# Kernel tuning notes

Hardware: AMD Instinct MI355X
Metric: run time of the kernel (lower is better)

Reference implementation:

```python
import jax, jax.numpy as jnp
import numpy as np

B, K, N, F = 32, 4, 512, 128


def setup_inputs() -> dict:
    key = jax.random.key(0)
    k1, k2, k3, k4 = jax.random.split(key, 4)
    H = jax.random.normal(k1, (B, N, F), dtype=jnp.float32)
    E = jax.random.uniform(k2, (B, K, N, N), dtype=jnp.float32)
    # xavier_normal_ equivalents
    rw_std = float(np.sqrt(2.0 / (F + F * K)))  # torch xavier treats last dims
    RW = jax.random.normal(k3, (F, F, K), dtype=jnp.float32) * rw_std
    sw_std = float(np.sqrt(2.0 / (F + F)))
    SW = jax.random.normal(k4, (F, F), dtype=jnp.float32) * sw_std
    return {"H": H, "E": E, "RW": RW, "SW": SW}


def reference(H, E, RW, SW):
    # D = 1 / sum over (k, i) of (E + I)  -> [b, n]
    n = E.shape[2]
    D = 1.0 / (E + jnp.eye(n, dtype=E.dtype)).sum(axis=(1, 2))  # [b, n]
    # relational aggregation: sum_{k,j,m} E[b,k,i,j] H[b,j,m] RW[m,f,k] -> [b,i,f]
    rel = jnp.einsum('bkij,bjm,mfk->bif', E, H, RW)
    self_term = jnp.einsum('bjf,fl->bjl', H, SW)
    return jax.nn.sigmoid(D[:, :, None] * rel + self_term)
```

## Files before the change

### kernel.cpp

```cpp
#include <hip/hip_runtime.h>
#include <hip/hip_bf16.h>

#define B_ 32
#define K_ 4
#define N_ 512
#define F_ 128

typedef __attribute__((ext_vector_type(8))) short short8;
typedef __attribute__((ext_vector_type(4))) short short4v;
typedef __attribute__((ext_vector_type(4))) float float4v;

__device__ __forceinline__ unsigned short f2bf(float x) {
    unsigned int u = __builtin_bit_cast(unsigned int, x);
    u += 0x7FFFu + ((u >> 16) & 1u);
    return (unsigned short)(u >> 16);
}

__device__ __forceinline__ short8 pack8(float4v a, float4v b) {
    short8 r;
    r[0] = (short)f2bf(a[0]); r[1] = (short)f2bf(a[1]);
    r[2] = (short)f2bf(a[2]); r[3] = (short)f2bf(a[3]);
    r[4] = (short)f2bf(b[0]); r[5] = (short)f2bf(b[1]);
    r[6] = (short)f2bf(b[2]); r[7] = (short)f2bf(b[3]);
    return r;
}

__global__ void k0_weights(const float* __restrict__ RW, const float* __restrict__ SW,
                           unsigned short* __restrict__ Wt, unsigned short* __restrict__ SWt) {
    int r = blockIdx.x;
    int m = threadIdx.x;
    if (r < 512) {
        int k = r >> 7, f = r & 127;
        Wt[r * F_ + m] = f2bf(RW[(m * F_ + f) * K_ + k]);
    } else {
        int l = r - 512;
        SWt[l * F_ + m] = f2bf(SW[m * F_ + l]);
    }
}

__global__ void k1v2_convert(const float* __restrict__ E, float* __restrict__ colsum,
                             unsigned short* __restrict__ Ebf) {
    int bid = blockIdx.x;
    int b   = bid >> 5;
    int isl = (bid >> 1) & 15;
    int jt  = bid & 1;
    int t   = threadIdx.x;
    int j   = jt * 256 + (t & 63) * 4;
    int r0  = isl * 32 + (t >> 6) * 8;

    float cs0 = 0.f, cs1 = 0.f, cs2 = 0.f, cs3 = 0.f;
#pragma unroll
    for (int k = 0; k < K_; ++k) {
        const float* Ep = E + ((size_t)((b * K_ + k) * N_ + r0)) * N_ + j;
        unsigned short* Op = Ebf + ((size_t)((b * K_ + k) * N_ + r0)) * N_ + j;
#pragma unroll
        for (int r = 0; r < 8; ++r) {
            float4v v = *(const float4v*)(Ep + (size_t)r * N_);
            cs0 += v[0]; cs1 += v[1]; cs2 += v[2]; cs3 += v[3];
            short4v s;
            s[0] = (short)f2bf(v[0]); s[1] = (short)f2bf(v[1]);
            s[2] = (short)f2bf(v[2]); s[3] = (short)f2bf(v[3]);
            *(short4v*)(Op + (size_t)r * N_) = s;
        }
    }
    atomicAdd(&colsum[b * N_ + j + 0], cs0);
    atomicAdd(&colsum[b * N_ + j + 1], cs1);
    atomicAdd(&colsum[b * N_ + j + 2], cs2);
    atomicAdd(&colsum[b * N_ + j + 3], cs3);
}

__global__ void k2_expand(const float* __restrict__ H, const unsigned short* __restrict__ Wt,
                          unsigned short* __restrict__ Tt) {
    int bid = blockIdx.x;
    int b  = bid >> 5;
    int ct = (bid >> 2) & 7;
    int jt = bid & 3;
    int lane = threadIdx.x & 63;
    int wv   = threadIdx.x >> 6;
    int c0 = ct * 64 + wv * 16;
    int jbase = jt * 128;
    int lrow = lane & 15, lgrp = lane >> 4;

    float4v acc[8];
#pragma unroll
    for (int i = 0; i < 8; ++i) acc[i] = {0.f, 0.f, 0.f, 0.f};

#pragma unroll
    for (int ms = 0; ms < 4; ++ms) {
        int m0 = ms * 32;
        short8 a = *(const short8*)(Wt + (c0 + lrow) * F_ + m0 + lgrp * 8);
#pragma unroll
        for (int cf = 0; cf < 8; ++cf) {
            int j = jbase + cf * 16 + lrow;
            const float* hp = H + ((size_t)b * N_ + j) * F_ + m0 + lgrp * 8;
            float4v h0 = *(const float4v*)hp;
            float4v h1 = *(const float4v*)(hp + 4);
            short8 bb = pack8(h0, h1);
            acc[cf] = __builtin_amdgcn_mfma_f32_16x16x32_bf16(a, bb, acc[cf], 0, 0, 0);
        }
    }
#pragma unroll
    for (int cf = 0; cf < 8; ++cf) {
#pragma unroll
        for (int r = 0; r < 4; ++r) {
            int c = c0 + lgrp * 4 + r;
            int j = jbase + cf * 16 + lrow;
            Tt[((size_t)b * 512 + c) * N_ + j] = f2bf(acc[cf][r]);
        }
    }
}

__global__ void __launch_bounds__(512)
k3v2_rel(const unsigned short* __restrict__ Ebf, const unsigned short* __restrict__ Tt,
         float* __restrict__ relP) {
    int bid = blockIdx.x;
    int b  = bid >> 4;
    int it = (bid >> 1) & 7;
    int jc = bid & 1;
    int lane = threadIdx.x & 63;
    int wv   = threadIdx.x >> 6;
    int i0 = it * 64 + (wv >> 1) * 16;
    int f0 = (wv & 1) * 64;
    int lrow = lane & 15, lgrp = lane >> 4;
    int jbase = jc * 256;

    float4v acc[4];
#pragma unroll
    for (int i = 0; i < 4; ++i) acc[i] = {0.f, 0.f, 0.f, 0.f};

    const unsigned short* Eb = Ebf + ((size_t)(b * K_) * N_ + (i0 + lrow)) * N_ + jbase + lgrp * 8;
    const unsigned short* Tb = Tt + ((size_t)b * 512 + f0 + lrow) * N_ + jbase + lgrp * 8;

#define EA(t) (const short8*)(Eb + ((t) >> 3) * 262144 + ((t) & 7) * 32)
#define TA(t, cf) (const short8*)(Tb + ((t) >> 3) * 65536 + (cf) * 8192 + ((t) & 7) * 32)

    short8 a0, b00, b01, b02, b03;
    short8 a1, b10, b11, b12, b13;
    a0 = *EA(0); b00 = *TA(0, 0); b01 = *TA(0, 1); b02 = *TA(0, 2); b03 = *TA(0, 3);

    for (int t = 0; t < 32; t += 2) {
        int t1 = t + 1;
        int t2 = (t + 2 < 32) ? t + 2 : 31;
        a1 = *EA(t1); b10 = *TA(t1, 0); b11 = *TA(t1, 1); b12 = *TA(t1, 2); b13 = *TA(t1, 3);
        acc[0] = __builtin_amdgcn_mfma_f32_16x16x32_bf16(a0, b00, acc[0], 0, 0, 0);
        acc[1] = __builtin_amdgcn_mfma_f32_16x16x32_bf16(a0, b01, acc[1], 0, 0, 0);
        acc[2] = __builtin_amdgcn_mfma_f32_16x16x32_bf16(a0, b02, acc[2], 0, 0, 0);
        acc[3] = __builtin_amdgcn_mfma_f32_16x16x32_bf16(a0, b03, acc[3], 0, 0, 0);
        a0 = *EA(t2); b00 = *TA(t2, 0); b01 = *TA(t2, 1); b02 = *TA(t2, 2); b03 = *TA(t2, 3);
        acc[0] = __builtin_amdgcn_mfma_f32_16x16x32_bf16(a1, b10, acc[0], 0, 0, 0);
        acc[1] = __builtin_amdgcn_mfma_f32_16x16x32_bf16(a1, b11, acc[1], 0, 0, 0);
        acc[2] = __builtin_amdgcn_mfma_f32_16x16x32_bf16(a1, b12, acc[2], 0, 0, 0);
        acc[3] = __builtin_amdgcn_mfma_f32_16x16x32_bf16(a1, b13, acc[3], 0, 0, 0);
    }
#undef EA
#undef TA

    float* dst = relP + (size_t)jc * (B_ * N_ * F_);
#pragma unroll
    for (int cf = 0; cf < 4; ++cf) {
#pragma unroll
        for (int r = 0; r < 4; ++r) {
            int i = i0 + lgrp * 4 + r;
            int f = f0 + cf * 16 + lrow;
            dst[((size_t)b * N_ + i) * F_ + f] = acc[cf][r];
        }
    }
}

__global__ void __launch_bounds__(512)
k4_epi(const float* __restrict__ relP, const float* __restrict__ H,
       const unsigned short* __restrict__ SWt, const float* __restrict__ colsum,
       float* __restrict__ out) {
    int bid = blockIdx.x;
    int b  = bid >> 3;
    int it = bid & 7;
    int lane = threadIdx.x & 63;
    int wv   = threadIdx.x >> 6;
    int i0 = it * 64 + (wv >> 1) * 16;
    int f0 = (wv & 1) * 64;
    int lrow = lane & 15, lgrp = lane >> 4;

    float4v accS[4];
#pragma unroll
    for (int i = 0; i < 4; ++i) accS[i] = {0.f, 0.f, 0.f, 0.f};

    const float* Hp = H + ((size_t)b * N_ + i0 + lrow) * F_;
#pragma unroll
    for (int ms = 0; ms < 4; ++ms) {
        int m0 = ms * 32;
        const float* hp = Hp + m0 + lgrp * 8;
        float4v h0 = *(const float4v*)hp;
        float4v h1 = *(const float4v*)(hp + 4);
        short8 a = pack8(h0, h1);
#pragma unroll
        for (int cf = 0; cf < 4; ++cf) {
            const unsigned short* sp = SWt + (f0 + cf * 16 + lrow) * F_ + m0 + lgrp * 8;
            short8 bb = *(const short8*)sp;
            accS[cf] = __builtin_amdgcn_mfma_f32_16x16x32_bf16(a, bb, accS[cf], 0, 0, 0);
        }
    }

    float Dv[4];
#pragma unroll
    for (int r = 0; r < 4; ++r) {
        int i = i0 + lgrp * 4 + r;
        Dv[r] = 1.0f / (colsum[b * N_ + i] + (float)K_);
    }
#pragma unroll
    for (int cf = 0; cf < 4; ++cf) {
#pragma unroll
        for (int r = 0; r < 4; ++r) {
            int i = i0 + lgrp * 4 + r;
            int f = f0 + cf * 16 + lrow;
            size_t idx = ((size_t)b * N_ + i) * F_ + f;
            float v = relP[idx] + relP[idx + (size_t)B_ * N_ * F_];
            float x = Dv[r] * v + accS[cf][r];
            out[idx] = 1.0f / (1.0f + __expf(-x));
        }
    }
}

__global__ void k1_colsum(const float* __restrict__ E, float* __restrict__ colsum) {
    int bid = blockIdx.x;
    int b   = bid >> 5;
    int jt  = (bid >> 4) & 1;
    int isl = bid & 15;
    int j   = jt * 256 + threadIdx.x;
    int i0  = isl * 32;
    float s0 = 0.f, s1 = 0.f, s2 = 0.f, s3 = 0.f;
#pragma unroll
    for (int k = 0; k < K_; ++k) {
        const float* p = E + ((size_t)((b * K_ + k) * N_ + i0)) * N_ + j;
#pragma unroll 4
        for (int ii = 0; ii < 32; ii += 4) {
            s0 += p[(ii + 0) * N_];
            s1 += p[(ii + 1) * N_];
            s2 += p[(ii + 2) * N_];
            s3 += p[(ii + 3) * N_];
        }
    }
    atomicAdd(&colsum[b * N_ + j], (s0 + s1) + (s2 + s3));
}

__global__ void __launch_bounds__(512)
k3_fuse(const float* __restrict__ E, const float* __restrict__ H,
        const unsigned short* __restrict__ Tt, const unsigned short* __restrict__ SWt,
        const float* __restrict__ colsum, float* __restrict__ out) {
    int bid = blockIdx.x;
    int b  = bid >> 3;
    int it = bid & 7;
    int lane = threadIdx.x & 63;
    int wv   = threadIdx.x >> 6;
    int i0 = it * 64 + (wv >> 1) * 16;
    int f0 = (wv & 1) * 64;
    int lrow = lane & 15, lgrp = lane >> 4;

    float4v accR[4], accS[4];
#pragma unroll
    for (int i = 0; i < 4; ++i) { accR[i] = {0.f, 0.f, 0.f, 0.f}; accS[i] = {0.f, 0.f, 0.f, 0.f}; }

    for (int k = 0; k < K_; ++k) {
        const float* Eb = E + ((size_t)((b * K_ + k) * N_ + i0 + lrow)) * N_;
        const unsigned short* Tb = Tt + ((size_t)b * 512 + k * 128 + f0) * N_;
#pragma unroll 2
        for (int js = 0; js < 16; ++js) {
            int j0 = js * 32;
            const float* ep = Eb + j0 + lgrp * 8;
            float4v e0 = *(const float4v*)ep;
            float4v e1 = *(const float4v*)(ep + 4);
            short8 a = pack8(e0, e1);
#pragma unroll
            for (int cf = 0; cf < 4; ++cf) {
                const unsigned short* tp = Tb + (size_t)(cf * 16 + lrow) * N_ + j0 + lgrp * 8;
                short8 bb = *(const short8*)tp;
                accR[cf] = __builtin_amdgcn_mfma_f32_16x16x32_bf16(a, bb, accR[cf], 0, 0, 0);
            }
        }
    }
    {
        const float* Hp = H + ((size_t)b * N_ + i0 + lrow) * F_;
#pragma unroll
        for (int ms = 0; ms < 4; ++ms) {
            int m0 = ms * 32;
            const float* hp = Hp + m0 + lgrp * 8;
            float4v h0 = *(const float4v*)hp;
            float4v h1 = *(const float4v*)(hp + 4);
            short8 a = pack8(h0, h1);
#pragma unroll
            for (int cf = 0; cf < 4; ++cf) {
                const unsigned short* sp = SWt + (f0 + cf * 16 + lrow) * F_ + m0 + lgrp * 8;
                short8 bb = *(const short8*)sp;
                accS[cf] = __builtin_amdgcn_mfma_f32_16x16x32_bf16(a, bb, accS[cf], 0, 0, 0);
            }
        }
    }
    float Dv[4];
#pragma unroll
    for (int r = 0; r < 4; ++r) {
        int i = i0 + lgrp * 4 + r;
        Dv[r] = 1.0f / (colsum[b * N_ + i] + (float)K_);
    }
#pragma unroll
    for (int cf = 0; cf < 4; ++cf) {
#pragma unroll
        for (int r = 0; r < 4; ++r) {
            int i = i0 + lgrp * 4 + r;
            int f = f0 + cf * 16 + lrow;
            float x = Dv[r] * accR[cf][r] + accS[cf][r];
            out[((size_t)b * N_ + i) * F_ + f] = 1.0f / (1.0f + __expf(-x));
        }
    }
}

extern "C" void kernel_launch(void* const* d_in, const int* in_sizes, int n_in,
                              void* d_out, int out_size, void* d_ws, size_t ws_size,
                              hipStream_t stream) {
    const float* H  = (const float*)d_in[0];
    const float* E  = (const float*)d_in[1];
    const float* RW = (const float*)d_in[2];
    const float* SW = (const float*)d_in[3];
    float* out = (float*)d_out;

    char* ws = (char*)d_ws;
    unsigned short* Wt  = (unsigned short*)(ws);
    unsigned short* SWt = (unsigned short*)(ws + 131072);
    float* colsum       = (float*)(ws + 163840);
    unsigned short* Tt  = (unsigned short*)(ws + 262144);
    unsigned short* Ebf = (unsigned short*)(ws + 17039360);
    float* relP         = (float*)(ws + 84148224);
    const size_t WS_NEED = 100925440ull;

    hipMemsetAsync(colsum, 0, B_ * N_ * sizeof(float), stream);
    k0_weights<<<640, 128, 0, stream>>>(RW, SW, Wt, SWt);

    if (ws_size >= WS_NEED) {
        k1v2_convert<<<1024, 256, 0, stream>>>(E, colsum, Ebf);
        k2_expand<<<1024, 256, 0, stream>>>(H, Wt, Tt);
        k3v2_rel<<<512, 512, 0, stream>>>(Ebf, Tt, relP);
        k4_epi<<<256, 512, 0, stream>>>(relP, H, SWt, colsum, out);
    } else {
        k1_colsum<<<1024, 256, 0, stream>>>(E, colsum);
        k2_expand<<<1024, 256, 0, stream>>>(H, Wt, Tt);
        k3_fuse<<<256, 512, 0, stream>>>(E, H, Tt, SWt, colsum, out);
    }
}
```

Before: 339.8 us.

## Widen E conversion per thread, split rel GEMM over four j-chunks

Result: no change. 342.2 us (+0.7%).

```diff
diff --git a/kernel.cpp b/kernel.cpp
--- a/kernel.cpp
+++ b/kernel.cpp
@@ -38,39 +38,59 @@
     }
 }
 
-__global__ void k1v2_convert(const float* __restrict__ E, float* __restrict__ colsum,
-                             unsigned short* __restrict__ Ebf) {
-    int bid = blockIdx.x;
-    int b   = bid >> 5;
-    int isl = (bid >> 1) & 15;
-    int jt  = bid & 1;
+__global__ void __launch_bounds__(256)
+k1v3_convert(const float* __restrict__ E, float* __restrict__ colsum,
+             unsigned short* __restrict__ Ebf) {
+    int bid = blockIdx.x;
+    int b   = bid >> 6;
+    int k   = (bid >> 4) & 3;
+    int isl = bid & 15;
     int t   = threadIdx.x;
-    int j   = jt * 256 + (t & 63) * 4;
+    int j8  = (t & 63) * 8;
     int r0  = isl * 32 + (t >> 6) * 8;
 
-    float cs0 = 0.f, cs1 = 0.f, cs2 = 0.f, cs3 = 0.f;
-#pragma unroll
-    for (int k = 0; k < K_; ++k) {
-        const float* Ep = E + ((size_t)((b * K_ + k) * N_ + r0)) * N_ + j;
-        unsigned short* Op = Ebf + ((size_t)((b * K_ + k) * N_ + r0)) * N_ + j;
-#pragma unroll
-        for (int r = 0; r < 8; ++r) {
-            float4v v = *(const float4v*)(Ep + (size_t)r * N_);
-            cs0 += v[0]; cs1 += v[1]; cs2 += v[2]; cs3 += v[3];
-            short4v s;
-            s[0] = (short)f2bf(v[0]); s[1] = (short)f2bf(v[1]);
-            s[2] = (short)f2bf(v[2]); s[3] = (short)f2bf(v[3]);
-            *(short4v*)(Op + (size_t)r * N_) = s;
-        }
-    }
-    atomicAdd(&colsum[b * N_ + j + 0], cs0);
-    atomicAdd(&colsum[b * N_ + j + 1], cs1);
-    atomicAdd(&colsum[b * N_ + j + 2], cs2);
-    atomicAdd(&colsum[b * N_ + j + 3], cs3);
-}
-
-__global__ void k2_expand(const float* __restrict__ H, const unsigned short* __restrict__ Wt,
-                          unsigned short* __restrict__ Tt) {
+    const size_t base = ((size_t)((b * K_ + k) * N_ + r0)) * N_ + j8;
+    const float* Ep = E + base;
+    unsigned short* Op = Ebf + base;
+
+    float4v va[8], vb[8];
+#pragma unroll
+    for (int r = 0; r < 4; ++r) {
+        va[r] = *(const float4v*)(Ep + (size_t)r * N_);
+        vb[r] = *(const float4v*)(Ep + (size_t)r * N_ + 4);
+    }
+#pragma unroll
+    for (int r = 4; r < 8; ++r) {
+        va[r] = *(const float4v*)(Ep + (size_t)r * N_);
+        vb[r] = *(const float4v*)(Ep + (size_t)r * N_ + 4);
+    }
+
+    float cs[8];
+#pragma unroll
+    for (int e = 0; e < 8; ++e) cs[e] = 0.f;
+#pragma unroll
+    for (int r = 0; r < 8; ++r) {
+        cs[0] += va[r][0]; cs[1] += va[r][1]; cs[2] += va[r][2]; cs[3] += va[r][3];
+        cs[4] += vb[r][0]; cs[5] += vb[r][1]; cs[6] += vb[r][2]; cs[7] += vb[r][3];
+        *(short8*)(Op + (size_t)r * N_) = pack8(va[r], vb[r]);
+    }
+
+    __shared__ float red[256][9];
+#pragma unroll
+    for (int e = 0; e < 8; ++e) red[t][e] = cs[e];
+    __syncthreads();
+    if (t < 64) {
+#pragma unroll
+        for (int e = 0; e < 8; ++e) {
+            float s = red[t][e] + red[t + 64][e] + red[t + 128][e] + red[t + 192][e];
+            atomicAdd(&colsum[b * N_ + t * 8 + e], s);
+        }
+    }
+}
+
+__global__ void __launch_bounds__(256)
+k2v2_expand(const float* __restrict__ H, const unsigned short* __restrict__ Wt,
+            unsigned short* __restrict__ Tt) {
     int bid = blockIdx.x;
     int b  = bid >> 5;
     int ct = (bid >> 2) & 7;
@@ -89,13 +109,16 @@
     for (int ms = 0; ms < 4; ++ms) {
         int m0 = ms * 32;
         short8 a = *(const short8*)(Wt + (c0 + lrow) * F_ + m0 + lgrp * 8);
+        float4v hv0[8], hv1[8];
 #pragma unroll
         for (int cf = 0; cf < 8; ++cf) {
-            int j = jbase + cf * 16 + lrow;
-            const float* hp = H + ((size_t)b * N_ + j) * F_ + m0 + lgrp * 8;
-            float4v h0 = *(const float4v*)hp;
-            float4v h1 = *(const float4v*)(hp + 4);
-            short8 bb = pack8(h0, h1);
+            const float* hp = H + ((size_t)b * N_ + jbase + cf * 16 + lrow) * F_ + m0 + lgrp * 8;
+            hv0[cf] = *(const float4v*)hp;
+            hv1[cf] = *(const float4v*)(hp + 4);
+        }
+#pragma unroll
+        for (int cf = 0; cf < 8; ++cf) {
+            short8 bb = pack8(hv0[cf], hv1[cf]);
             acc[cf] = __builtin_amdgcn_mfma_f32_16x16x32_bf16(a, bb, acc[cf], 0, 0, 0);
         }
     }
@@ -111,18 +134,18 @@
 }
 
 __global__ void __launch_bounds__(512)
-k3v2_rel(const unsigned short* __restrict__ Ebf, const unsigned short* __restrict__ Tt,
+k3v3_rel(const unsigned short* __restrict__ Ebf, const unsigned short* __restrict__ Tt,
          float* __restrict__ relP) {
     int bid = blockIdx.x;
-    int b  = bid >> 4;
-    int it = (bid >> 1) & 7;
-    int jc = bid & 1;
+    int b  = bid >> 5;
+    int it = (bid >> 2) & 7;
+    int jc = bid & 3;
     int lane = threadIdx.x & 63;
     int wv   = threadIdx.x >> 6;
     int i0 = it * 64 + (wv >> 1) * 16;
     int f0 = (wv & 1) * 64;
     int lrow = lane & 15, lgrp = lane >> 4;
-    int jbase = jc * 256;
+    int jbase = jc * 128;
 
     float4v acc[4];
 #pragma unroll
@@ -131,16 +154,16 @@
     const unsigned short* Eb = Ebf + ((size_t)(b * K_) * N_ + (i0 + lrow)) * N_ + jbase + lgrp * 8;
     const unsigned short* Tb = Tt + ((size_t)b * 512 + f0 + lrow) * N_ + jbase + lgrp * 8;
 
-#define EA(t) (const short8*)(Eb + ((t) >> 3) * 262144 + ((t) & 7) * 32)
-#define TA(t, cf) (const short8*)(Tb + ((t) >> 3) * 65536 + (cf) * 8192 + ((t) & 7) * 32)
+#define EA(t) (const short8*)(Eb + ((t) >> 2) * 262144 + ((t) & 3) * 32)
+#define TA(t, cf) (const short8*)(Tb + ((t) >> 2) * 65536 + (cf) * 8192 + ((t) & 3) * 32)
 
     short8 a0, b00, b01, b02, b03;
     short8 a1, b10, b11, b12, b13;
     a0 = *EA(0); b00 = *TA(0, 0); b01 = *TA(0, 1); b02 = *TA(0, 2); b03 = *TA(0, 3);
 
-    for (int t = 0; t < 32; t += 2) {
+    for (int t = 0; t < 16; t += 2) {
         int t1 = t + 1;
-        int t2 = (t + 2 < 32) ? t + 2 : 31;
+        int t2 = (t + 2 < 16) ? t + 2 : 15;
         a1 = *EA(t1); b10 = *TA(t1, 0); b11 = *TA(t1, 1); b12 = *TA(t1, 2); b13 = *TA(t1, 3);
         acc[0] = __builtin_amdgcn_mfma_f32_16x16x32_bf16(a0, b00, acc[0], 0, 0, 0);
         acc[1] = __builtin_amdgcn_mfma_f32_16x16x32_bf16(a0, b01, acc[1], 0, 0, 0);
@@ -206,6 +229,7 @@
         int i = i0 + lgrp * 4 + r;
         Dv[r] = 1.0f / (colsum[b * N_ + i] + (float)K_);
     }
+    const size_t S = (size_t)B_ * N_ * F_;
 #pragma unroll
     for (int cf = 0; cf < 4; ++cf) {
 #pragma unroll
@@ -213,7 +237,7 @@
             int i = i0 + lgrp * 4 + r;
             int f = f0 + cf * 16 + lrow;
             size_t idx = ((size_t)b * N_ + i) * F_ + f;
-            float v = relP[idx] + relP[idx + (size_t)B_ * N_ * F_];
+            float v = relP[idx] + relP[idx + S] + relP[idx + 2 * S] + relP[idx + 3 * S];
             float x = Dv[r] * v + accS[cf][r];
             out[idx] = 1.0f / (1.0f + __expf(-x));
         }
@@ -328,19 +352,19 @@
     unsigned short* Tt  = (unsigned short*)(ws + 262144);
     unsigned short* Ebf = (unsigned short*)(ws + 17039360);
     float* relP         = (float*)(ws + 84148224);
-    const size_t WS_NEED = 100925440ull;
+    const size_t WS_NEED = 117702656ull;
 
     hipMemsetAsync(colsum, 0, B_ * N_ * sizeof(float), stream);
     k0_weights<<<640, 128, 0, stream>>>(RW, SW, Wt, SWt);
 
     if (ws_size >= WS_NEED) {
-        k1v2_convert<<<1024, 256, 0, stream>>>(E, colsum, Ebf);
-        k2_expand<<<1024, 256, 0, stream>>>(H, Wt, Tt);
-        k3v2_rel<<<512, 512, 0, stream>>>(Ebf, Tt, relP);
+        k1v3_convert<<<2048, 256, 0, stream>>>(E, colsum, Ebf);
+        k2v2_expand<<<1024, 256, 0, stream>>>(H, Wt, Tt);
+        k3v3_rel<<<1024, 512, 0, stream>>>(Ebf, Tt, relP);
         k4_epi<<<256, 512, 0, stream>>>(relP, H, SWt, colsum, out);
     } else {
         k1_colsum<<<1024, 256, 0, stream>>>(E, colsum);
-        k2_expand<<<1024, 256, 0, stream>>>(H, Wt, Tt);
+        k2v2_expand<<<1024, 256, 0, stream>>>(H, Wt, Tt);
         k3_fuse<<<256, 512, 0, stream>>>(E, H, Tt, SWt, colsum, out);
     }
 }
```
